# Kernel tuning notes

Hardware: AMD Instinct MI355X
Metric: run time of the kernel (lower is better)

Reference implementation:

```python
import jax, jax.numpy as jnp
import numpy as np
from jax import lax

B, N, D = 32, 131072, 3
NUM_POINTS = 1024  # K = min(num_points, N)
INF = 1e10


def setup_inputs() -> dict:
    key = jax.random.key(0)
    k1, k2 = jax.random.split(key)
    points = jax.random.normal(k1, (B, N, D), dtype=jnp.float32)
    init_idx = jax.random.randint(k2, (B,), 0, N, dtype=jnp.int32)
    return {"points": points, "init_idx": init_idx}


def reference(points, init_idx):
    """Farthest point sampling: returns (B, K, D) sampled points."""
    b, n, d = points.shape
    K = min(NUM_POINTS, n)
    xyz = points[:, :, :3]  # distances use first 3 coords only

    def step(carry, _):
        dist, last = carry  # dist: (B, N), last: (B,)
        last_pt = jnp.take_along_axis(xyz, last[:, None, None], axis=1)  # (B,1,3)
        d2 = jnp.sum((xyz - last_pt) ** 2, axis=-1)  # (B, N)
        dist = jnp.minimum(dist, d2)
        nxt = jnp.argmax(dist, axis=-1).astype(last.dtype)  # (B,)
        return (dist, nxt), nxt

    dist0 = jnp.full((b, n), INF, dtype=points.dtype)
    init = init_idx.astype(jnp.int32)
    (_, _), rest = lax.scan(step, (dist0, init), None, length=K - 1)  # rest: (K-1, B)
    centroids = jnp.concatenate([init[:, None], rest.T], axis=1)  # (B, K)
    # gather sampled points: (B, K, D)
    return jnp.take_along_axis(points, centroids[:, :, None], axis=1)
```

## Files before the change

### kernel.cpp

```cpp
#include <hip/hip_runtime.h>
#include <stdint.h>

typedef unsigned long long u64;

#define BATCH 32
#define NPTS  131072
#define KOUT  1024
#define NBLK  8
#define TPB   512
#define PPT   (NPTS / (NBLK * TPB))
#define NWAVES (TPB / 64)

struct __align__(32) Slot {
    u64 w0;
    u64 w1;
    u64 w2;
    u64 pad;
};

__global__ __launch_bounds__(TPB, 2) void fps_kernel(
    const float* __restrict__ points,
    const int*   __restrict__ init_idx,
    float*       __restrict__ out,
    Slot*        __restrict__ slots)
{
    const int gid = blockIdx.x;
    const int b   = (gid >> 6) * 8 + (gid & 7);
    const int blk = (gid & 63) >> 3;
    const int tid = threadIdx.x;
    const float* bp = points + (size_t)b * NPTS * 3;

    float  px[PPT], py[PPT], pz[PPT];
    double dist[PPT];
    const int nbase = blk * (NPTS / NBLK) + tid;
#pragma unroll
    for (int j = 0; j < PPT; ++j) {
        int n = nbase + j * TPB;
        px[j]   = bp[(size_t)n * 3 + 0];
        py[j]   = bp[(size_t)n * 3 + 1];
        pz[j]   = bp[(size_t)n * 3 + 2];
        dist[j] = 1e10;
    }
#pragma unroll
    for (int j = 0; j < PPT; ++j) {
        asm volatile("" : "+v"(px[j]), "+v"(py[j]), "+v"(pz[j]));
    }

    __shared__ float  s_last[3];
    __shared__ double s_wd[NWAVES];
    __shared__ int    s_wi[NWAVES];

    const int last = init_idx[b];
    if (blk == 0 && tid < 3) {
        out[((size_t)b * KOUT) * 3 + tid] = bp[(size_t)last * 3 + tid];
    }
    float lx = bp[(size_t)last * 3 + 0];
    float ly = bp[(size_t)last * 3 + 1];
    float lz = bp[(size_t)last * 3 + 2];

    for (int it = 0; it < KOUT - 1; ++it) {
        const double lxd = (double)lx, lyd = (double)ly, lzd = (double)lz;

        double bestd = -1.0;
        int    besti = 0;
#pragma unroll
        for (int j = 0; j < PPT; ++j) {
            double dx = (double)px[j] - lxd;
            double dy = (double)py[j] - lyd;
            double dz = (double)pz[j] - lzd;
            double d2 = dx * dx + dy * dy + dz * dz;
            double nd = fmin(dist[j], d2);
            dist[j] = nd;
            if (nd > bestd) { bestd = nd; besti = nbase + j * TPB; }
        }

#pragma unroll
        for (int off = 32; off > 0; off >>= 1) {
            double od = __shfl_xor(bestd, off, 64);
            int    oi = __shfl_xor(besti, off, 64);
            if (od > bestd || (od == bestd && oi < besti)) { bestd = od; besti = oi; }
        }
        const int wid  = tid >> 6;
        const int lane = tid & 63;
        if (lane == 0) { s_wd[wid] = bestd; s_wi[wid] = besti; }
        __syncthreads();

        const u64  r  = (u64)(uint32_t)(it + 1);
        const u64  rh = r << 32;
        Slot* sb = &slots[((size_t)(it & 1) * BATCH + b) * NBLK];

        if (wid == 0) {
            double vd = -1.0; int vi = 0x7FFFFFFF;
            if (lane < NWAVES) { vd = s_wd[lane]; vi = s_wi[lane]; }
#pragma unroll
            for (int off = 4; off > 0; off >>= 1) {
                double od = __shfl_xor(vd, off, 64);
                int    oi = __shfl_xor(vi, off, 64);
                if (od > vd || (od == vd && oi < vi)) { vd = od; vi = oi; }
            }
            if (lane == 0) {
                Slot* s = sb + blk;
                u64 d64 = (u64)__double_as_longlong(vd);
                __hip_atomic_store(&s->w0, rh | (d64 >> 32),
                                   __ATOMIC_RELAXED, __HIP_MEMORY_SCOPE_AGENT);
                __hip_atomic_store(&s->w1, rh | (d64 & 0xFFFFFFFFull),
                                   __ATOMIC_RELAXED, __HIP_MEMORY_SCOPE_AGENT);
                __hip_atomic_store(&s->w2, rh | (u64)(uint32_t)vi,
                                   __ATOMIC_RELAXED, __HIP_MEMORY_SCOPE_AGENT);
            }
            if (lane < NBLK) {
                Slot* s = sb + lane;
                u64 a, c, d;
                do {
                    a = __hip_atomic_load(&s->w0, __ATOMIC_RELAXED, __HIP_MEMORY_SCOPE_AGENT);
                    c = __hip_atomic_load(&s->w1, __ATOMIC_RELAXED, __HIP_MEMORY_SCOPE_AGENT);
                    d = __hip_atomic_load(&s->w2, __ATOMIC_RELAXED, __HIP_MEMORY_SCOPE_AGENT);
                } while ((a >> 32) != r || (c >> 32) != r || (d >> 32) != r);
                u64 gd = (a << 32) | (c & 0xFFFFFFFFull);
                int gi = (int)(uint32_t)d;
                float gx = bp[(size_t)gi * 3 + 0];
                float gy = bp[(size_t)gi * 3 + 1];
                float gz = bp[(size_t)gi * 3 + 2];
#pragma unroll
                for (int off = 4; off > 0; off >>= 1) {
                    u64   od = (u64)__shfl_xor((long long)gd, off, 64);
                    int   oi = __shfl_xor(gi, off, 64);
                    float ox = __shfl_xor(gx, off, 64);
                    float oy = __shfl_xor(gy, off, 64);
                    float oz = __shfl_xor(gz, off, 64);
                    if (od > gd || (od == gd && oi < gi)) {
                        gd = od; gi = oi; gx = ox; gy = oy; gz = oz;
                    }
                }
                if (lane == 0) {
                    s_last[0] = gx; s_last[1] = gy; s_last[2] = gz;
                    if (blk == 0) {
                        size_t o_ = ((size_t)b * KOUT + (it + 1)) * 3;
                        out[o_ + 0] = gx; out[o_ + 1] = gy; out[o_ + 2] = gz;
                    }
                }
            }
        }
        __syncthreads();
        lx = s_last[0]; ly = s_last[1]; lz = s_last[2];
    }
}

extern "C" void kernel_launch(void* const* d_in, const int* in_sizes, int n_in,
                              void* d_out, int out_size, void* d_ws, size_t ws_size,
                              hipStream_t stream) {
    const float* points   = (const float*)d_in[0];
    const int*   init_idx = (const int*)d_in[1];
    float*       out      = (float*)d_out;
    Slot*        slots    = (Slot*)d_ws;

    void* args[] = { (void*)&points, (void*)&init_idx, (void*)&out, (void*)&slots };
    hipLaunchCooperativeKernel((const void*)fps_kernel,
                               dim3(BATCH * NBLK), dim3(TPB),
                               args, 0, stream);
}
```

Baseline: 5.257 ms.

## Replace block barriers with per-wave global slot exchange across blocks

Each wave now publishes its own argmax candidate to a global slot (64 slots per batch), and every wave polls all 64 slots itself and reduces them with a 64-lane shuffle. This removes both __syncthreads barriers and the shared-memory handoff, so waves advance independently. In exchange it adds 8x more global polling traffic and atomic loads per iteration. The workspace must also be large enough for the larger slot array.

After: 9.885 ms. +88.0%, slower.

```diff
diff --git a/kernel.cpp b/kernel.cpp
--- a/kernel.cpp
+++ b/kernel.cpp
@@ -10,6 +10,7 @@
 #define TPB   512
 #define PPT   (NPTS / (NBLK * TPB))
 #define NWAVES (TPB / 64)
+#define NSLOT  (NBLK * NWAVES)
 
 struct __align__(32) Slot {
     u64 w0;
@@ -28,6 +29,8 @@
     const int b   = (gid >> 6) * 8 + (gid & 7);
     const int blk = (gid & 63) >> 3;
     const int tid = threadIdx.x;
+    const int wid  = tid >> 6;
+    const int lane = tid & 63;
     const float* bp = points + (size_t)b * NPTS * 3;
 
     float  px[PPT], py[PPT], pz[PPT];
@@ -46,10 +49,6 @@
         asm volatile("" : "+v"(px[j]), "+v"(py[j]), "+v"(pz[j]));
     }
 
-    __shared__ float  s_last[3];
-    __shared__ double s_wd[NWAVES];
-    __shared__ int    s_wi[NWAVES];
-
     const int last = init_idx[b];
     if (blk == 0 && tid < 3) {
         out[((size_t)b * KOUT) * 3 + tid] = bp[(size_t)last * 3 + tid];
@@ -57,6 +56,8 @@
     float lx = bp[(size_t)last * 3 + 0];
     float ly = bp[(size_t)last * 3 + 1];
     float lz = bp[(size_t)last * 3 + 2];
+
+    const int myslot = blk * NWAVES + wid;
 
     for (int it = 0; it < KOUT - 1; ++it) {
         const double lxd = (double)lx, lyd = (double)ly, lzd = (double)lz;
@@ -80,69 +81,53 @@
             int    oi = __shfl_xor(besti, off, 64);
             if (od > bestd || (od == bestd && oi < besti)) { bestd = od; besti = oi; }
         }
-        const int wid  = tid >> 6;
-        const int lane = tid & 63;
-        if (lane == 0) { s_wd[wid] = bestd; s_wi[wid] = besti; }
-        __syncthreads();
 
-        const u64  r  = (u64)(uint32_t)(it + 1);
-        const u64  rh = r << 32;
-        Slot* sb = &slots[((size_t)(it & 1) * BATCH + b) * NBLK];
+        const u64 r  = (u64)(uint32_t)(it + 1);
+        const u64 rh = r << 32;
+        Slot* sb = &slots[((size_t)(it & 1) * BATCH + b) * NSLOT];
 
-        if (wid == 0) {
-            double vd = -1.0; int vi = 0x7FFFFFFF;
-            if (lane < NWAVES) { vd = s_wd[lane]; vi = s_wi[lane]; }
+        if (lane == 0) {
+            Slot* s = sb + myslot;
+            u64 d64 = (u64)__double_as_longlong(bestd);
+            __hip_atomic_store(&s->w0, rh | (d64 >> 32),
+                               __ATOMIC_RELAXED, __HIP_MEMORY_SCOPE_AGENT);
+            __hip_atomic_store(&s->w1, rh | (d64 & 0xFFFFFFFFull),
+                               __ATOMIC_RELAXED, __HIP_MEMORY_SCOPE_AGENT);
+            __hip_atomic_store(&s->w2, rh | (u64)(uint32_t)besti,
+                               __ATOMIC_RELAXED, __HIP_MEMORY_SCOPE_AGENT);
+        }
+        asm volatile("s_waitcnt vmcnt(0)" ::: "memory");
+
+        {
+            Slot* s = sb + lane;
+            u64 a, c, d;
+            do {
+                a = __hip_atomic_load(&s->w0, __ATOMIC_RELAXED, __HIP_MEMORY_SCOPE_AGENT);
+                c = __hip_atomic_load(&s->w1, __ATOMIC_RELAXED, __HIP_MEMORY_SCOPE_AGENT);
+                d = __hip_atomic_load(&s->w2, __ATOMIC_RELAXED, __HIP_MEMORY_SCOPE_AGENT);
+            } while (((a >> 32) != r) | ((c >> 32) != r) | ((d >> 32) != r));
+            u64 gd = (a << 32) | (c & 0xFFFFFFFFull);
+            int gi = (int)(uint32_t)d;
+            float gx = bp[(size_t)gi * 3 + 0];
+            float gy = bp[(size_t)gi * 3 + 1];
+            float gz = bp[(size_t)gi * 3 + 2];
 #pragma unroll
-            for (int off = 4; off > 0; off >>= 1) {
-                double od = __shfl_xor(vd, off, 64);
-                int    oi = __shfl_xor(vi, off, 64);
-                if (od > vd || (od == vd && oi < vi)) { vd = od; vi = oi; }
-            }
-            if (lane == 0) {
-                Slot* s = sb + blk;
-                u64 d64 = (u64)__double_as_longlong(vd);
-                __hip_atomic_store(&s->w0, rh | (d64 >> 32),
-                                   __ATOMIC_RELAXED, __HIP_MEMORY_SCOPE_AGENT);
-                __hip_atomic_store(&s->w1, rh | (d64 & 0xFFFFFFFFull),
-                                   __ATOMIC_RELAXED, __HIP_MEMORY_SCOPE_AGENT);
-                __hip_atomic_store(&s->w2, rh | (u64)(uint32_t)vi,
-                                   __ATOMIC_RELAXED, __HIP_MEMORY_SCOPE_AGENT);
-            }
-            if (lane < NBLK) {
-                Slot* s = sb + lane;
-                u64 a, c, d;
-                do {
-                    a = __hip_atomic_load(&s->w0, __ATOMIC_RELAXED, __HIP_MEMORY_SCOPE_AGENT);
-                    c = __hip_atomic_load(&s->w1, __ATOMIC_RELAXED, __HIP_MEMORY_SCOPE_AGENT);
-                    d = __hip_atomic_load(&s->w2, __ATOMIC_RELAXED, __HIP_MEMORY_SCOPE_AGENT);
-                } while ((a >> 32) != r || (c >> 32) != r || (d >> 32) != r);
-                u64 gd = (a << 32) | (c & 0xFFFFFFFFull);
-                int gi = (int)(uint32_t)d;
-                float gx = bp[(size_t)gi * 3 + 0];
-                float gy = bp[(size_t)gi * 3 + 1];
-                float gz = bp[(size_t)gi * 3 + 2];
-#pragma unroll
-                for (int off = 4; off > 0; off >>= 1) {
-                    u64   od = (u64)__shfl_xor((long long)gd, off, 64);
-                    int   oi = __shfl_xor(gi, off, 64);
-                    float ox = __shfl_xor(gx, off, 64);
-                    float oy = __shfl_xor(gy, off, 64);
-                    float oz = __shfl_xor(gz, off, 64);
-                    if (od > gd || (od == gd && oi < gi)) {
-                        gd = od; gi = oi; gx = ox; gy = oy; gz = oz;
-                    }
-                }
-                if (lane == 0) {
-                    s_last[0] = gx; s_last[1] = gy; s_last[2] = gz;
-                    if (blk == 0) {
-                        size_t o_ = ((size_t)b * KOUT + (it + 1)) * 3;
-                        out[o_ + 0] = gx; out[o_ + 1] = gy; out[o_ + 2] = gz;
-                    }
+            for (int off = 32; off > 0; off >>= 1) {
+                u64   od = (u64)__shfl_xor((long long)gd, off, 64);
+                int   oi = __shfl_xor(gi, off, 64);
+                float ox = __shfl_xor(gx, off, 64);
+                float oy = __shfl_xor(gy, off, 64);
+                float oz = __shfl_xor(gz, off, 64);
+                if (od > gd || (od == gd && oi < gi)) {
+                    gd = od; gi = oi; gx = ox; gy = oy; gz = oz;
                 }
             }
+            lx = gx; ly = gy; lz = gz;
+            if (blk == 0 && tid == 0) {
+                size_t o_ = ((size_t)b * KOUT + (it + 1)) * 3;
+                out[o_ + 0] = gx; out[o_ + 1] = gy; out[o_ + 2] = gz;
+            }
         }
-        __syncthreads();
-        lx = s_last[0]; ly = s_last[1]; lz = s_last[2];
     }
 }
 
```

## Replace per-iteration __syncthreads with LDS tag flags between waves

Applied to the files above, without the earlier changes.

Removes both workgroup barriers per iteration and replaces them with tagged LDS mailboxes. Each wave publishes its partial argmax with a release store and wave 0 spins on the tags. The other waves spin on an output tag to receive the next centroid, and wave 0 now uses its full 8-lane group to poll the cross-block slots. The goal is to cut barrier latency on the serial 1023-iteration critical path, at the cost of spin-wait contention on LDS and a risk of subtle ordering bugs. Because tags are iteration-numbered, a slow wave could in principle see its s_in slot overwritten before wave 0 reads it, though the output tag wait prevents this.

New measurement: 5.750 ms. +9.4%, slower.

```diff
diff --git a/kernel.cpp b/kernel.cpp
--- a/kernel.cpp
+++ b/kernel.cpp
@@ -28,6 +28,8 @@
     const int b   = (gid >> 6) * 8 + (gid & 7);
     const int blk = (gid & 63) >> 3;
     const int tid = threadIdx.x;
+    const int wid  = tid >> 6;
+    const int lane = tid & 63;
     const float* bp = points + (size_t)b * NPTS * 3;
 
     float  px[PPT], py[PPT], pz[PPT];
@@ -46,9 +48,15 @@
         asm volatile("" : "+v"(px[j]), "+v"(py[j]), "+v"(pz[j]));
     }
 
-    __shared__ float  s_last[3];
-    __shared__ double s_wd[NWAVES];
-    __shared__ int    s_wi[NWAVES];
+    __shared__ u64      s_in_d[NWAVES];
+    __shared__ int      s_in_i[NWAVES];
+    __shared__ uint32_t s_in_tag[NWAVES];
+    __shared__ float    s_out_x, s_out_y, s_out_z;
+    __shared__ uint32_t s_out_tag;
+
+    if (tid < NWAVES) s_in_tag[tid] = 0;
+    if (tid == 0)     s_out_tag = 0;
+    __syncthreads();
 
     const int last = init_idx[b];
     if (blk == 0 && tid < 3) {
@@ -80,69 +88,85 @@
             int    oi = __shfl_xor(besti, off, 64);
             if (od > bestd || (od == bestd && oi < besti)) { bestd = od; besti = oi; }
         }
-        const int wid  = tid >> 6;
-        const int lane = tid & 63;
-        if (lane == 0) { s_wd[wid] = bestd; s_wi[wid] = besti; }
-        __syncthreads();
 
-        const u64  r  = (u64)(uint32_t)(it + 1);
-        const u64  rh = r << 32;
-        Slot* sb = &slots[((size_t)(it & 1) * BATCH + b) * NBLK];
+        const uint32_t r = (uint32_t)(it + 1);
 
+        if (lane == 0) {
+            s_in_d[wid] = (u64)__double_as_longlong(bestd);
+            s_in_i[wid] = besti;
+            __hip_atomic_store(&s_in_tag[wid], r, __ATOMIC_RELEASE,
+                               __HIP_MEMORY_SCOPE_WORKGROUP);
+        }
+
+        float gx, gy, gz;
         if (wid == 0) {
-            double vd = -1.0; int vi = 0x7FFFFFFF;
-            if (lane < NWAVES) { vd = s_wd[lane]; vi = s_wi[lane]; }
+            const int src = lane & 7;
+            uint32_t t;
+            do {
+                t = __hip_atomic_load(&s_in_tag[src], __ATOMIC_ACQUIRE,
+                                      __HIP_MEMORY_SCOPE_WORKGROUP);
+            } while (t != r);
+            u64 vd = s_in_d[src];
+            int vi = s_in_i[src];
 #pragma unroll
             for (int off = 4; off > 0; off >>= 1) {
-                double od = __shfl_xor(vd, off, 64);
-                int    oi = __shfl_xor(vi, off, 64);
+                u64 od = (u64)__shfl_xor((long long)vd, off, 64);
+                int oi = __shfl_xor(vi, off, 64);
                 if (od > vd || (od == vd && oi < vi)) { vd = od; vi = oi; }
             }
+            const u64 rh = (u64)r << 32;
+            Slot* sb = &slots[((size_t)(it & 1) * BATCH + b) * NBLK];
             if (lane == 0) {
                 Slot* s = sb + blk;
-                u64 d64 = (u64)__double_as_longlong(vd);
-                __hip_atomic_store(&s->w0, rh | (d64 >> 32),
+                __hip_atomic_store(&s->w0, rh | (vd >> 32),
                                    __ATOMIC_RELAXED, __HIP_MEMORY_SCOPE_AGENT);
-                __hip_atomic_store(&s->w1, rh | (d64 & 0xFFFFFFFFull),
+                __hip_atomic_store(&s->w1, rh | (vd & 0xFFFFFFFFull),
                                    __ATOMIC_RELAXED, __HIP_MEMORY_SCOPE_AGENT);
                 __hip_atomic_store(&s->w2, rh | (u64)(uint32_t)vi,
                                    __ATOMIC_RELAXED, __HIP_MEMORY_SCOPE_AGENT);
             }
-            if (lane < NBLK) {
-                Slot* s = sb + lane;
-                u64 a, c, d;
-                do {
-                    a = __hip_atomic_load(&s->w0, __ATOMIC_RELAXED, __HIP_MEMORY_SCOPE_AGENT);
-                    c = __hip_atomic_load(&s->w1, __ATOMIC_RELAXED, __HIP_MEMORY_SCOPE_AGENT);
-                    d = __hip_atomic_load(&s->w2, __ATOMIC_RELAXED, __HIP_MEMORY_SCOPE_AGENT);
-                } while ((a >> 32) != r || (c >> 32) != r || (d >> 32) != r);
-                u64 gd = (a << 32) | (c & 0xFFFFFFFFull);
-                int gi = (int)(uint32_t)d;
-                float gx = bp[(size_t)gi * 3 + 0];
-                float gy = bp[(size_t)gi * 3 + 1];
-                float gz = bp[(size_t)gi * 3 + 2];
+            asm volatile("s_waitcnt vmcnt(0)" ::: "memory");
+            Slot* s = sb + src;
+            u64 a, c, d;
+            do {
+                a = __hip_atomic_load(&s->w0, __ATOMIC_RELAXED, __HIP_MEMORY_SCOPE_AGENT);
+                c = __hip_atomic_load(&s->w1, __ATOMIC_RELAXED, __HIP_MEMORY_SCOPE_AGENT);
+                d = __hip_atomic_load(&s->w2, __ATOMIC_RELAXED, __HIP_MEMORY_SCOPE_AGENT);
+            } while (((a >> 32) != r) | ((c >> 32) != r) | ((d >> 32) != r));
+            u64 gd = (a << 32) | (c & 0xFFFFFFFFull);
+            int gi = (int)(uint32_t)d;
+            gx = bp[(size_t)gi * 3 + 0];
+            gy = bp[(size_t)gi * 3 + 1];
+            gz = bp[(size_t)gi * 3 + 2];
 #pragma unroll
-                for (int off = 4; off > 0; off >>= 1) {
-                    u64   od = (u64)__shfl_xor((long long)gd, off, 64);
-                    int   oi = __shfl_xor(gi, off, 64);
-                    float ox = __shfl_xor(gx, off, 64);
-                    float oy = __shfl_xor(gy, off, 64);
-                    float oz = __shfl_xor(gz, off, 64);
-                    if (od > gd || (od == gd && oi < gi)) {
-                        gd = od; gi = oi; gx = ox; gy = oy; gz = oz;
-                    }
-                }
-                if (lane == 0) {
-                    s_last[0] = gx; s_last[1] = gy; s_last[2] = gz;
-                    if (blk == 0) {
-                        size_t o_ = ((size_t)b * KOUT + (it + 1)) * 3;
-                        out[o_ + 0] = gx; out[o_ + 1] = gy; out[o_ + 2] = gz;
-                    }
+            for (int off = 4; off > 0; off >>= 1) {
+                u64   od = (u64)__shfl_xor((long long)gd, off, 64);
+                int   oi = __shfl_xor(gi, off, 64);
+                float ox = __shfl_xor(gx, off, 64);
+                float oy = __shfl_xor(gy, off, 64);
+                float oz = __shfl_xor(gz, off, 64);
+                if (od > gd || (od == gd && oi < gi)) {
+                    gd = od; gi = oi; gx = ox; gy = oy; gz = oz;
                 }
             }
+            if (lane == 0) {
+                s_out_x = gx; s_out_y = gy; s_out_z = gz;
+                __hip_atomic_store(&s_out_tag, r, __ATOMIC_RELEASE,
+                                   __HIP_MEMORY_SCOPE_WORKGROUP);
+                if (blk == 0) {
+                    size_t o_ = ((size_t)b * KOUT + (it + 1)) * 3;
+                    out[o_ + 0] = gx; out[o_ + 1] = gy; out[o_ + 2] = gz;
+                }
+            }
+        } else {
+            uint32_t t;
+            do {
+                t = __hip_atomic_load(&s_out_tag, __ATOMIC_ACQUIRE,
+                                      __HIP_MEMORY_SCOPE_WORKGROUP);
+            } while (t != r);
+            gx = s_out_x; gy = s_out_y; gz = s_out_z;
         }
-        __syncthreads();
-        lx = s_last[0]; ly = s_last[1]; lz = s_last[2];
+        lx = gx; ly = gy; lz = gz;
     }
 }
 
```
